# Kernel tuning notes

Hardware: AMD Instinct MI355X
Metric: run time of the kernel (lower is better)

Reference implementation:

```python
import jax, jax.numpy as jnp
import numpy as np

BASELINE = 0.24  # vertical stereo baseline used in the original forward


def setup_inputs() -> dict:
    key = jax.random.key(0)
    k1, k2, k3 = jax.random.split(key, 3)
    bs, C, H, W = 1, 16, 256, 512
    ndisp = 32
    x = jax.random.normal(k1, (bs, C, H, W), dtype=jnp.float32)
    y = jax.random.normal(k2, (bs, C, H, W), dtype=jnp.float32)
    depth = jax.random.uniform(k3, (bs, ndisp, H, W), dtype=jnp.float32,
                               minval=0.5, maxval=8.0)
    return {"x": x, "y": y, "depth_range_samples": depth, "ndisp": ndisp}


def _theta_rows(height):
    # spherical latitude per pixel row (equirectangular, pixel-centered),
    # theta in (-pi/2, pi/2) -- S360.grid.create_spherical_grid channel 1
    v = (jnp.arange(height, dtype=jnp.float32) + 0.5) * (np.pi / height) - np.pi / 2
    return v[None, None, :, None]  # [1,1,H,1]


def _dtheta_vertical(theta, depth, baseline, height):
    # S360.derivatives.dtheta_vertical: angular shift of a scene point at
    # (theta, depth) seen from a camera displaced vertically by `baseline`,
    # converted from radians to pixel rows.
    dth = jnp.arctan((depth * jnp.sin(theta) + baseline) / (depth * jnp.cos(theta))) - theta
    return dth * (height / np.pi)


def _grid_sample_bilinear_zeros(img, grid):
    # Faithful F.grid_sample(mode='bilinear', padding_mode='zeros',
    # align_corners=False). img [B,C,H,W]; grid [B,Hg,Wg,2] in [-1,1].
    B, C, H, W = img.shape
    ix = ((grid[..., 0] + 1.0) * W - 1.0) * 0.5  # unnormalize (align_corners=False)
    iy = ((grid[..., 1] + 1.0) * H - 1.0) * 0.5
    x0 = jnp.floor(ix)
    y0 = jnp.floor(iy)
    wx1 = ix - x0
    wy1 = iy - y0
    img_flat = img.reshape(B, C, H * W)

    def corner(xi, yi, w):
        valid = (xi >= 0) & (xi <= W - 1) & (yi >= 0) & (yi <= H - 1)
        xc = jnp.clip(xi, 0, W - 1).astype(jnp.int32)
        yc = jnp.clip(yi, 0, H - 1).astype(jnp.int32)
        flat = yc * W + xc                                   # [B,Hg,Wg]
        v = jax.vmap(lambda im, f: im[:, f])(img_flat, flat)  # [B,C,Hg,Wg]
        return v * (w * valid.astype(img.dtype))[:, None]

    return (corner(x0,     y0,     (1 - wx1) * (1 - wy1))
          + corner(x0 + 1, y0,     wx1       * (1 - wy1))
          + corner(x0,     y0 + 1, (1 - wx1) * wy1)
          + corner(x0 + 1, y0 + 1, wx1       * wy1))


def reference(x, y, depth_range_samples, ndisp):
    bs, C, H, W = x.shape
    theta = _theta_rows(H)                                   # [1,1,H,1]
    d_v = _dtheta_vertical(theta, depth_range_samples, BASELINE, H)  # [bs,nd,H,W]
    v = jnp.arange(H, dtype=x.dtype)[None, None, :, None]
    u = jnp.arange(W, dtype=x.dtype)[None, None, None, :]
    # torch zeroes NaN/Inf entries of (uvgrid + disp); x-coords (disp_x=0) stay u
    y_px = jnp.where(jnp.isfinite(d_v), v + d_v, 0.0)        # [bs,nd,H,W]
    coords_x = jnp.broadcast_to(u / ((W - 1.0) / 2.0) - 1.0, y_px.shape)
    coords_y = y_px / ((H - 1.0) / 2.0) - 1.0
    grid = jnp.stack([coords_x, coords_y], axis=-1)          # [bs,nd,H,W,2]
    warped = _grid_sample_bilinear_zeros(y, grid.reshape(bs, ndisp * H, W, 2))
    warped = warped.reshape(bs, C, ndisp, H, W)
    ref = jnp.broadcast_to(x[:, :, None], (bs, C, ndisp, H, W))
    return jnp.concatenate([ref, warped], axis=1)            # [bs,2C,nd,H,W]
```

## Files before the change

kernel.cpp:

```cpp
#include <hip/hip_runtime.h>
#include <math.h>

#define CCH 16
#define HH 256
#define WW 512
#define ND 32
#define HWSZ (HH * WW)
#define BASELINE 0.24f

__global__ __launch_bounds__(256) void transpose_y_kernel(
    const float* __restrict__ y, float* __restrict__ yt)
{
    int p = blockIdx.x * blockDim.x + threadIdx.x;
    if (p >= HWSZ) return;
    float v[CCH];
    #pragma unroll
    for (int c = 0; c < CCH; ++c) v[c] = y[c * HWSZ + p];
    float4* dst = (float4*)(yt + (size_t)p * CCH);
    #pragma unroll
    for (int j = 0; j < 4; ++j)
        dst[j] = make_float4(v[4 * j], v[4 * j + 1], v[4 * j + 2], v[4 * j + 3]);
}

__global__ __launch_bounds__(256) void cost_volume_kernel(
    const float* __restrict__ x,
    const float4* __restrict__ yt4,
    const float* __restrict__ depth,
    float* __restrict__ out)
{
    int w = blockIdx.x * 64 + (threadIdx.x & 63);
    int h = blockIdx.y;
    int d = blockIdx.z * 4 + (threadIdx.x >> 6);
    int p = h * WW + w;

    float dep = depth[d * HWSZ + p];

    float theta = ((float)h + 0.5f) * (float)(M_PI / HH) - (float)(M_PI / 2.0);
    float st, ct;
    sincosf(theta, &st, &ct);

    float dth = atanf((dep * st + BASELINE) / (dep * ct)) - theta;
    float d_v = dth * (float)(HH / M_PI);
    float y_px = isfinite(d_v) ? ((float)h + d_v) : 0.0f;

    float cx = (float)w / ((WW - 1.0f) * 0.5f) - 1.0f;
    float cy = y_px   / ((HH - 1.0f) * 0.5f) - 1.0f;
    float ix = ((cx + 1.0f) * (float)WW - 1.0f) * 0.5f;
    float iy = ((cy + 1.0f) * (float)HH - 1.0f) * 0.5f;

    float x0f = floorf(ix);
    float y0f = floorf(iy);
    float wx1 = ix - x0f;
    float wy1 = iy - y0f;
    float wx0 = 1.0f - wx1;
    float wy0 = 1.0f - wy1;

    int x0 = (int)x0f;
    int y0 = (int)y0f;
    int x1 = x0 + 1;
    int y1 = y0 + 1;

    float vx0 = (x0 >= 0 && x0 <= WW - 1) ? 1.0f : 0.0f;
    float vx1 = (x1 >= 0 && x1 <= WW - 1) ? 1.0f : 0.0f;
    float vy0 = (y0 >= 0 && y0 <= HH - 1) ? 1.0f : 0.0f;
    float vy1 = (y1 >= 0 && y1 <= HH - 1) ? 1.0f : 0.0f;

    int x0c = min(max(x0, 0), WW - 1);
    int x1c = min(max(x1, 0), WW - 1);
    int y0c = min(max(y0, 0), HH - 1);
    int y1c = min(max(y1, 0), HH - 1);

    float w00 = wx0 * wy0 * vx0 * vy0;
    float w10 = wx1 * wy0 * vx1 * vy0;
    float w01 = wx0 * wy1 * vx0 * vy1;
    float w11 = wx1 * wy1 * vx1 * vy1;

    int b00 = (y0c * WW + x0c) * 4;
    int b10 = (y0c * WW + x1c) * 4;
    int b01 = (y1c * WW + x0c) * 4;
    int b11 = (y1c * WW + x1c) * 4;

    float4 acc[4];
    #pragma unroll
    for (int j = 0; j < 4; ++j) {
        float4 a = yt4[b00 + j];
        acc[j] = make_float4(a.x * w00, a.y * w00, a.z * w00, a.w * w00);
    }
    #pragma unroll
    for (int j = 0; j < 4; ++j) {
        float4 a = yt4[b10 + j];
        acc[j].x += a.x * w10; acc[j].y += a.y * w10;
        acc[j].z += a.z * w10; acc[j].w += a.w * w10;
    }
    #pragma unroll
    for (int j = 0; j < 4; ++j) {
        float4 a = yt4[b01 + j];
        acc[j].x += a.x * w01; acc[j].y += a.y * w01;
        acc[j].z += a.z * w01; acc[j].w += a.w * w01;
    }
    #pragma unroll
    for (int j = 0; j < 4; ++j) {
        float4 a = yt4[b11 + j];
        acc[j].x += a.x * w11; acc[j].y += a.y * w11;
        acc[j].z += a.z * w11; acc[j].w += a.w * w11;
    }

    const float* accf = (const float*)acc;
    size_t dp = (size_t)d * HWSZ + p;

    #pragma unroll
    for (int c = 0; c < CCH; ++c) {
        out[(size_t)c * (ND * HWSZ) + dp] = x[c * HWSZ + p];
        out[(size_t)(CCH + c) * (ND * HWSZ) + dp] = accf[c];
    }
}

extern "C" void kernel_launch(void* const* d_in, const int* in_sizes, int n_in,
                              void* d_out, int out_size, void* d_ws, size_t ws_size,
                              hipStream_t stream) {
    const float* x = (const float*)d_in[0];
    const float* y = (const float*)d_in[1];
    const float* depth = (const float*)d_in[2];
    float* out = (float*)d_out;
    float* yt = (float*)d_ws;

    transpose_y_kernel<<<(HWSZ + 255) / 256, 256, 0, stream>>>(y, yt);

    dim3 grid(WW / 64, HH, ND / 4);
    cost_volume_kernel<<<grid, 256, 0, stream>>>(x, (const float4*)yt, depth, out);
}
```

Before: 664.5 us.

## Split x broadcast into vectorized kernel and use nontemporal stores

Moves the broadcast of x into its own kernel, which loads each x vector once and writes it to all disparity slices with 16-byte nontemporal stores. The warp kernel now writes only the warped half, also with nontemporal stores, and reads depth with nontemporal loads. Its grid is reordered so that blocks adjacent in launch order cover different disparities of the same row. The aim is better write bandwidth and less cache pollution on a store-bound workload, at the cost of one extra kernel launch.

Measured after the change: 624.9 us. -6.0%, faster.

```diff
diff --git a/kernel.cpp b/kernel.cpp
--- a/kernel.cpp
+++ b/kernel.cpp
@@ -8,6 +8,8 @@
 #define HWSZ (HH * WW)
 #define BASELINE 0.24f
 
+typedef float f4 __attribute__((ext_vector_type(4)));
+
 __global__ __launch_bounds__(256) void transpose_y_kernel(
     const float* __restrict__ y, float* __restrict__ yt)
 {
@@ -16,24 +18,37 @@
     float v[CCH];
     #pragma unroll
     for (int c = 0; c < CCH; ++c) v[c] = y[c * HWSZ + p];
-    float4* dst = (float4*)(yt + (size_t)p * CCH);
+    f4* dst = (f4*)(yt + (size_t)p * CCH);
     #pragma unroll
-    for (int j = 0; j < 4; ++j)
-        dst[j] = make_float4(v[4 * j], v[4 * j + 1], v[4 * j + 2], v[4 * j + 3]);
+    for (int j = 0; j < 4; ++j) {
+        f4 t = { v[4 * j], v[4 * j + 1], v[4 * j + 2], v[4 * j + 3] };
+        dst[j] = t;
+    }
 }
 
-__global__ __launch_bounds__(256) void cost_volume_kernel(
-    const float* __restrict__ x,
+__global__ __launch_bounds__(256) void broadcast_x_kernel(
+    const f4* __restrict__ x4, f4* __restrict__ out4)
+{
+    int p4 = blockIdx.x * 256 + threadIdx.x;
+    int c  = blockIdx.y;
+    f4 v = __builtin_nontemporal_load(&x4[(size_t)c * (HWSZ / 4) + p4]);
+    f4* base = out4 + (size_t)c * (size_t)ND * (HWSZ / 4) + p4;
+    #pragma unroll
+    for (int d = 0; d < ND; ++d)
+        __builtin_nontemporal_store(v, base + (size_t)d * (HWSZ / 4));
+}
+
+__global__ __launch_bounds__(256) void warp_kernel(
     const float4* __restrict__ yt4,
     const float* __restrict__ depth,
     float* __restrict__ out)
 {
-    int w = blockIdx.x * 64 + (threadIdx.x & 63);
-    int h = blockIdx.y;
-    int d = blockIdx.z * 4 + (threadIdx.x >> 6);
+    int d = blockIdx.x * 4 + (threadIdx.x >> 6);
+    int w = blockIdx.y * 64 + (threadIdx.x & 63);
+    int h = blockIdx.z;
     int p = h * WW + w;
 
-    float dep = depth[d * HWSZ + p];
+    float dep = __builtin_nontemporal_load(&depth[d * HWSZ + p]);
 
     float theta = ((float)h + 0.5f) * (float)(M_PI / HH) - (float)(M_PI / 2.0);
     float st, ct;
@@ -110,8 +125,8 @@
 
     #pragma unroll
     for (int c = 0; c < CCH; ++c) {
-        out[(size_t)c * (ND * HWSZ) + dp] = x[c * HWSZ + p];
-        out[(size_t)(CCH + c) * (ND * HWSZ) + dp] = accf[c];
+        __builtin_nontemporal_store(
+            accf[c], &out[(size_t)(CCH + c) * ((size_t)ND * HWSZ) + dp]);
     }
 }
 
@@ -126,6 +141,11 @@
 
     transpose_y_kernel<<<(HWSZ + 255) / 256, 256, 0, stream>>>(y, yt);
 
-    dim3 grid(WW / 64, HH, ND / 4);
-    cost_volume_kernel<<<grid, 256, 0, stream>>>(x, (const float4*)yt, depth, out);
+    dim3 bgrid(HWSZ / 4 / 256, CCH, 1);
+    broadcast_x_kernel<<<bgrid, 256, 0, stream>>>(
+        (const f4*)x, (f4*)out);
+
+    dim3 wgrid(ND / 4, WW / 64, HH);
+    warp_kernel<<<wgrid, 256, 0, stream>>>(
+        (const float4*)yt, depth, out);
 }
```
